# Optimization experiments

Hardware: AMD Instinct MI355X
Metric: run time of the kernel (lower is better)

Reference implementation:

```python
import jax, jax.numpy as jnp
import numpy as np

H_HEADS = 8
DIM_HEAD = 64


def setup_inputs() -> dict:
    key = jax.random.key(0)
    ks = jax.random.split(key, 5)
    b, c, Hs, Ws = 16, 32, 128, 128
    qd = H_HEADS * c              # 256 (heads*c = Linear in_features)
    inner = H_HEADS * DIM_HEAD    # 512
    s = 0.02                      # keep logits in a sane range
    return {
        "x": jax.random.normal(ks[0], (b, c, Hs, Ws), jnp.float32),
        "Wq": jax.random.normal(ks[1], (inner, qd), jnp.float32) * s,
        "Wkv": jax.random.normal(ks[2], (2 * inner, qd), jnp.float32) * s,
        "Wout": jax.random.normal(ks[3], (qd, inner), jnp.float32) * s,
        "bout": jax.random.normal(ks[4], (qd,), jnp.float32) * s,
    }


def _proj(arg, W, bias=None):
    # apply_operator_or_ffn for nn.Linear:
    # rearrange '(b h) n d -> b d (h n)', Linear over last dim, then 'b d n -> b n d'
    B, n, d = arg.shape
    bp = B // H_HEADS
    t = arg.reshape(bp, H_HEADS, n, d)
    t = jnp.transpose(t, (0, 3, 1, 2)).reshape(bp, d, H_HEADS * n)  # [b', d, h*n]
    y = t @ W.T
    if bias is not None:
        y = y + bias
    return jnp.transpose(y, (0, 2, 1))  # [b', out_features, d]


def _split_heads(t):
    # 'b (h d) n -> (b h) d n'
    bp, hd, n = t.shape
    return t.reshape(bp, H_HEADS, hd // H_HEADS, n).reshape(bp * H_HEADS, hd // H_HEADS, n)


def reference(x, Wq, Wkv, Wout, bout):
    b, c = x.shape[0], x.shape[1]
    spatial = x.shape[2:]
    N = int(np.prod(spatial))
    scale = DIM_HEAD ** -0.5
    xf = x.reshape(b, c, N)
    q = _proj(xf, Wq)              # [b/h, inner, N]
    kv = _proj(xf, Wkv)            # [b/h, 2*inner, N]
    inner = q.shape[1]
    k, v = kv[:, :inner], kv[:, inner:]
    qh, kh, vh = _split_heads(q), _split_heads(k), _split_heads(v)  # [b, DIM_HEAD, N]
    sim = jnp.einsum('bin,bjn->bij', qh, kh) * scale                 # [b, dh, dh]
    attn = jax.nn.softmax(sim, axis=-1)
    out = jnp.einsum('bnj,bjd->bnd', attn, vh)                       # [b, dh, N]
    out = _proj(out, Wout, bout)                                     # [b/h, h*c, N]
    return out.reshape(b, c, *spatial)
```

## Files before the change

### kernel.cpp

```cpp
#include <hip/hip_runtime.h>
#include <cstdint>
#include <cstddef>

using u16 = unsigned short;
using u32 = unsigned int;

typedef __attribute__((ext_vector_type(8))) short bf16x8;
typedef __attribute__((ext_vector_type(16))) float f32x16;

__device__ __forceinline__ u16 f2bf(float f) {
  union { float f; u32 i; } x; x.f = f;
  u32 r = (x.i + 0x7FFFu + ((x.i >> 16) & 1u)) >> 16;
  return (u16)r;
}
__device__ __forceinline__ bf16x8 ldbf16x8(const u16* p) {
  union { uint4 u; bf16x8 v; } t;
  t.u = *(const uint4*)p;
  return t.v;
}

constexpr int NP = 16384;

constexpr size_t OFF_C   = 0;
constexpr size_t OFF_T   = 131072;
constexpr size_t OFF_AT  = 393216;
constexpr size_t OFF_WE  = 458752;
constexpr size_t OFF_MT  = 720896;
constexpr size_t OFF_MA  = 851968;
constexpr size_t OFF_XB  = 917504;
constexpr size_t OFF_XBT = 5111808;
constexpr size_t OFF_CP1 = 9306112;
constexpr size_t NEED1   = (OFF_CP1 + 2097152) * 4;
constexpr size_t OFF_CP2 = 851968;
constexpr size_t NEED2   = (OFF_CP2 + 6291456) * 4;

__global__ __launch_bounds__(256)
void k0_cvt(const float* __restrict__ x, u16* __restrict__ Xb,
            u16* __restrict__ XbT) {
  __shared__ float Fs[256 * 65];
  const int pc = blockIdx.x;
  const int g  = blockIdx.y;
  const int p0 = pc * 64;
  const float* __restrict__ Xg = x + (size_t)g * 256 * NP;
  u16* __restrict__ Xbg  = Xb  + (size_t)g * 256 * NP;
  u16* __restrict__ XbTg = XbT + (size_t)g * NP * 256;
  const int tid = threadIdx.x;
  const int f8i = tid & 7, rb = tid >> 3;
  for (int pass = 0; pass < 8; ++pass) {
    const int row = rb + pass * 32;
    const size_t e0 = (size_t)row * NP + p0 + f8i * 8;
    float4 a = *(const float4*)(Xg + e0);
    float4 b = *(const float4*)(Xg + e0 + 4);
    const float v[8] = {a.x, a.y, a.z, a.w, b.x, b.y, b.z, b.w};
    uint4 s;
    s.x = (u32)f2bf(v[0]) | ((u32)f2bf(v[1]) << 16);
    s.y = (u32)f2bf(v[2]) | ((u32)f2bf(v[3]) << 16);
    s.z = (u32)f2bf(v[4]) | ((u32)f2bf(v[5]) << 16);
    s.w = (u32)f2bf(v[6]) | ((u32)f2bf(v[7]) << 16);
    *(uint4*)(Xbg + e0) = s;
    float* d = &Fs[row * 65 + f8i * 8];
#pragma unroll
    for (int e = 0; e < 8; ++e) d[e] = v[e];
  }
  __syncthreads();
  const int p = tid & 63, grp = tid >> 6;
  u16* dst = XbTg + (size_t)(p0 + p) * 256 + grp * 64;
  for (int c = 0; c < 4; ++c) {
    u32 w[8];
#pragma unroll
    for (int q = 0; q < 8; ++q) {
      const int f = grp * 64 + c * 16 + q * 2;
      u32 lo = f2bf(Fs[f * 65 + p]);
      u32 hi = f2bf(Fs[(f + 1) * 65 + p]);
      w[q] = lo | (hi << 16);
    }
    uint4 s0 = {w[0], w[1], w[2], w[3]};
    uint4 s1 = {w[4], w[5], w[6], w[7]};
    *(uint4*)(dst + c * 16)     = s0;
    *(uint4*)(dst + c * 16 + 8) = s1;
  }
}

__global__ __launch_bounds__(256)
void k1_mfma(const u16* __restrict__ Xb, float* __restrict__ Cpart) {
  const int kc = blockIdx.x;
  const int tp = blockIdx.y;
  const int g  = blockIdx.z;
  const int ti = tp >> 2, tj = tp & 3;
  const int tid = threadIdx.x;
  const int w = tid >> 6, half = (tid >> 5) & 1, lc = tid & 31;
  const int qi = w >> 1, qj = w & 1;
  const u16* __restrict__ Xg = Xb + (size_t)g * 256 * NP;
  const u16* A = Xg + (size_t)(ti * 64 + qi * 32 + lc) * NP + kc * 1024 + half * 8;
  const u16* B = Xg + (size_t)(tj * 64 + qj * 32 + lc) * NP + kc * 1024 + half * 8;
  f32x16 acc;
#pragma unroll
  for (int i = 0; i < 16; ++i) acc[i] = 0.f;
#pragma unroll 4
  for (int s = 0; s < 64; ++s) {
    bf16x8 a = ldbf16x8(A + s * 16);
    bf16x8 b = ldbf16x8(B + s * 16);
    acc = __builtin_amdgcn_mfma_f32_32x32x16_bf16(a, b, acc, 0, 0, 0);
  }
  float* __restrict__ P = Cpart + (((size_t)g * 16 + tp) * 16 + kc) * 4096;
#pragma unroll
  for (int r = 0; r < 16; ++r) {
    const int row = qi * 32 + (r & 3) + 8 * (r >> 2) + 4 * half;
    const int col = qj * 32 + lc;
    P[row * 64 + col] = acc[r];
  }
}

__global__ __launch_bounds__(256)
void k1b_red(const float* __restrict__ Cpart, float* __restrict__ Cmat) {
  const int sl = blockIdx.x;
  const int tp = blockIdx.y;
  const int g  = blockIdx.z;
  const int ele = sl * 256 + threadIdx.x;
  const float* __restrict__ P =
      Cpart + (((size_t)g * 16 + tp) * 16) * 4096 + ele;
  float v = 0.f;
#pragma unroll
  for (int kc = 0; kc < 16; ++kc) v += P[(size_t)kc * 4096];
  const int ti = tp >> 2, tj = tp & 3;
  const int r64 = ele >> 6, c64 = ele & 63;
  Cmat[(size_t)g * 65536 + (size_t)(ti * 64 + r64) * 256 + tj * 64 + c64] = v;
}

__global__ __launch_bounds__(256)
void k1_gram(const float* __restrict__ x, float* __restrict__ Cpart) {
  __shared__ float As[32 * 132];
  __shared__ float Bs[32 * 132];
  const int kc = blockIdx.x, ty = blockIdx.y, g = blockIdx.z;
  const int i0 = (ty == 2) ? 128 : 0;
  const int j0 = (ty == 0) ? 0 : 128;
  const float* __restrict__ Xg = x + (size_t)g * 256 * NP;
  const int tid = threadIdx.x, lane = tid & 63, w = tid >> 6;
  const int wy = (w >> 1) * 64, wx = (w & 1) * 64;
  const int ly = (lane >> 3) * 8, lx = (lane & 7) * 8;
  float acc[8][8];
#pragma unroll
  for (int e = 0; e < 8; ++e)
#pragma unroll
    for (int f = 0; f < 8; ++f) acc[e][f] = 0.f;
  const int k8 = (tid & 3) * 8, rowb = tid >> 2, k0 = kc * 256;
  for (int s = 0; s < 8; ++s) {
    const int ks = k0 + s * 32;
#pragma unroll
    for (int pass = 0; pass < 2; ++pass) {
      const int row = rowb + pass * 64;
      const size_t ea = (size_t)(i0 + row) * NP + ks + k8;
      float4 a = *(const float4*)(Xg + ea);
      float4 b = *(const float4*)(Xg + ea + 4);
      As[(k8+0)*132+row]=a.x; As[(k8+1)*132+row]=a.y;
      As[(k8+2)*132+row]=a.z; As[(k8+3)*132+row]=a.w;
      As[(k8+4)*132+row]=b.x; As[(k8+5)*132+row]=b.y;
      As[(k8+6)*132+row]=b.z; As[(k8+7)*132+row]=b.w;
      const size_t eb = (size_t)(j0 + row) * NP + ks + k8;
      a = *(const float4*)(Xg + eb);
      b = *(const float4*)(Xg + eb + 4);
      Bs[(k8+0)*132+row]=a.x; Bs[(k8+1)*132+row]=a.y;
      Bs[(k8+2)*132+row]=a.z; Bs[(k8+3)*132+row]=a.w;
      Bs[(k8+4)*132+row]=b.x; Bs[(k8+5)*132+row]=b.y;
      Bs[(k8+6)*132+row]=b.z; Bs[(k8+7)*132+row]=b.w;
    }
    __syncthreads();
#pragma unroll 4
    for (int kk = 0; kk < 32; ++kk) {
      const float* ar = &As[kk * 132 + wy + ly];
      const float* br = &Bs[kk * 132 + wx + lx];
      float4 a0 = *(const float4*)(ar), a1 = *(const float4*)(ar + 4);
      float4 b0 = *(const float4*)(br), b1 = *(const float4*)(br + 4);
      const float av[8] = {a0.x,a0.y,a0.z,a0.w,a1.x,a1.y,a1.z,a1.w};
      const float bv[8] = {b0.x,b0.y,b0.z,b0.w,b1.x,b1.y,b1.z,b1.w};
#pragma unroll
      for (int e = 0; e < 8; ++e)
#pragma unroll
        for (int f = 0; f < 8; ++f) acc[e][f] += av[e] * bv[f];
    }
    __syncthreads();
  }
  float* __restrict__ P = Cpart + (((size_t)g * 3 + ty) * 64 + kc) * 16384;
#pragma unroll
  for (int e = 0; e < 8; ++e) {
    float* pr = P + (size_t)(wy + ly + e) * 128 + wx + lx;
    float4 s0 = {acc[e][0], acc[e][1], acc[e][2], acc[e][3]};
    float4 s1 = {acc[e][4], acc[e][5], acc[e][6], acc[e][7]};
    *(float4*)(pr)     = s0;
    *(float4*)(pr + 4) = s1;
  }
}

__global__ __launch_bounds__(256)
void k1b_reduce(const float* __restrict__ Cpart, float* __restrict__ Cmat) {
  const int sl = blockIdx.x, ty = blockIdx.y, g = blockIdx.z;
  const int ele = sl * 256 + threadIdx.x;
  const float* __restrict__ P =
      Cpart + (((size_t)g * 3 + ty) * 64) * 16384 + ele;
  float v = 0.f;
#pragma unroll 8
  for (int kc = 0; kc < 64; ++kc) v += P[(size_t)kc * 16384];
  const int i0 = (ty == 2) ? 128 : 0;
  const int j0 = (ty == 0) ? 0 : 128;
  const int i = ele >> 7, j = ele & 127;
  float* Cg = Cmat + (size_t)g * 65536;
  Cg[(size_t)(i0 + i) * 256 + (j0 + j)] = v;
  if (ty == 1) Cg[(size_t)(j0 + j) * 256 + (i0 + i)] = v;
}

__global__ __launch_bounds__(256)
void k1_gram_atomic(const float* __restrict__ x, float* __restrict__ Cmat) {
  __shared__ float As[32 * 132];
  __shared__ float Bs[32 * 132];
  const int kc = blockIdx.x, ty = blockIdx.y, g = blockIdx.z;
  const int i0 = (ty == 2) ? 128 : 0;
  const int j0 = (ty == 0) ? 0 : 128;
  const float* __restrict__ Xg = x + (size_t)g * 256 * NP;
  const int tid = threadIdx.x, lane = tid & 63, w = tid >> 6;
  const int wy = (w >> 1) * 64, wx = (w & 1) * 64;
  const int ly = (lane >> 3) * 8, lx = (lane & 7) * 8;
  float acc[8][8];
#pragma unroll
  for (int e = 0; e < 8; ++e)
#pragma unroll
    for (int f = 0; f < 8; ++f) acc[e][f] = 0.f;
  const int k8 = (tid & 3) * 8, rowb = tid >> 2, k0 = kc * 256;
  for (int s = 0; s < 8; ++s) {
    const int ks = k0 + s * 32;
#pragma unroll
    for (int pass = 0; pass < 2; ++pass) {
      const int row = rowb + pass * 64;
      const size_t ea = (size_t)(i0 + row) * NP + ks + k8;
      float4 a = *(const float4*)(Xg + ea);
      float4 b = *(const float4*)(Xg + ea + 4);
      As[(k8+0)*132+row]=a.x; As[(k8+1)*132+row]=a.y;
      As[(k8+2)*132+row]=a.z; As[(k8+3)*132+row]=a.w;
      As[(k8+4)*132+row]=b.x; As[(k8+5)*132+row]=b.y;
      As[(k8+6)*132+row]=b.z; As[(k8+7)*132+row]=b.w;
      const size_t eb = (size_t)(j0 + row) * NP + ks + k8;
      a = *(const float4*)(Xg + eb);
      b = *(const float4*)(Xg + eb + 4);
      Bs[(k8+0)*132+row]=a.x; Bs[(k8+1)*132+row]=a.y;
      Bs[(k8+2)*132+row]=a.z; Bs[(k8+3)*132+row]=a.w;
      Bs[(k8+4)*132+row]=b.x; Bs[(k8+5)*132+row]=b.y;
      Bs[(k8+6)*132+row]=b.z; Bs[(k8+7)*132+row]=b.w;
    }
    __syncthreads();
#pragma unroll 4
    for (int kk = 0; kk < 32; ++kk) {
      const float* ar = &As[kk * 132 + wy + ly];
      const float* br = &Bs[kk * 132 + wx + lx];
      float4 a0 = *(const float4*)(ar), a1 = *(const float4*)(ar + 4);
      float4 b0 = *(const float4*)(br), b1 = *(const float4*)(br + 4);
      const float av[8] = {a0.x,a0.y,a0.z,a0.w,a1.x,a1.y,a1.z,a1.w};
      const float bv[8] = {b0.x,b0.y,b0.z,b0.w,b1.x,b1.y,b1.z,b1.w};
#pragma unroll
      for (int e = 0; e < 8; ++e)
#pragma unroll
        for (int f = 0; f < 8; ++f) acc[e][f] += av[e] * bv[f];
    }
    __syncthreads();
  }
  float* Cg = Cmat + (size_t)g * 65536;
#pragma unroll
  for (int e = 0; e < 8; ++e)
#pragma unroll
    for (int f = 0; f < 8; ++f) {
      atomicAdd(&Cg[(i0+wy+ly+e)*256 + (j0+wx+lx+f)], acc[e][f]);
      if (ty == 1)
        atomicAdd(&Cg[(j0+wx+lx+f)*256 + (i0+wy+ly+e)], acc[e][f]);
    }
}

__global__ __launch_bounds__(256)
void kA_attn(const float* __restrict__ Wq, const float* __restrict__ Wkv,
             const float* __restrict__ Cmat, float* __restrict__ attn) {
  __shared__ float WqL[4 * 256];
  __shared__ float Ts[4 * 256];
  const int bh = blockIdx.x;
  const int ic = blockIdx.y;
  const int g = bh >> 3, hh = bh & 7;
  const int tid = threadIdx.x;
  const float* __restrict__ Cg = Cmat + (size_t)g * 65536;
  {
    const int r = tid >> 6, c4 = (tid & 63) * 4;
    *(float4*)(&WqL[r * 256 + c4]) =
        *(const float4*)(Wq + (size_t)(hh * 64 + ic * 4 + r) * 256 + c4);
  }
  __syncthreads();
  float acc[4] = {0.f, 0.f, 0.f, 0.f};
#pragma unroll 8
  for (int b = 0; b < 256; ++b) {
    const float cv = Cg[(size_t)b * 256 + tid];
#pragma unroll
    for (int r = 0; r < 4; ++r) acc[r] += WqL[r * 256 + b] * cv;
  }
#pragma unroll
  for (int r = 0; r < 4; ++r) Ts[r * 256 + tid] = acc[r];
  __syncthreads();
  const int r = tid >> 6, j = tid & 63;
  const float* __restrict__ Wk = Wkv + (size_t)(hh * 64 + j) * 256;
  float s = 0.f;
#pragma unroll 4
  for (int a4 = 0; a4 < 64; ++a4) {
    float4 w = *(const float4*)(Wk + a4 * 4);
    const float* t4 = &Ts[r * 256 + a4 * 4];
    s += t4[0] * w.x + t4[1] * w.y + t4[2] * w.z + t4[3] * w.w;
  }
  s *= 0.125f;
  float m = s;
#pragma unroll
  for (int off = 32; off; off >>= 1) m = fmaxf(m, __shfl_xor(m, off));
  const float e = __expf(s - m);
  float sum = e;
#pragma unroll
  for (int off = 32; off; off >>= 1) sum += __shfl_xor(sum, off);
  attn[((size_t)bh * 64 + ic * 4 + r) * 64 + j] = e / sum;
}

__global__ __launch_bounds__(256)
void kB_m(const float* __restrict__ Wout, const float* __restrict__ Wkv,
          const float* __restrict__ attn, float* __restrict__ Mp) {
  __shared__ float AtL[64 * 64];
  __shared__ float WoL[16 * 64];
  __shared__ float UL[16 * 64];
  const int bh = blockIdx.x;
  const int cc = blockIdx.y;
  const int g = bh >> 3, hh = bh & 7;
  const int tid = threadIdx.x;
  {
    const float* __restrict__ A = attn + (size_t)bh * 4096;
#pragma unroll
    for (int q = 0; q < 4; ++q)
      *(float4*)(&AtL[q * 1024 + tid * 4]) =
          *(const float4*)(A + q * 1024 + tid * 4);
  }
  {
    const int co_l = tid >> 4, i4 = (tid & 15) * 4;
    *(float4*)(&WoL[co_l * 64 + i4]) =
        *(const float4*)(Wout + (size_t)(cc * 16 + co_l) * 512 + hh * 64 + i4);
  }
  __syncthreads();
  const int j = tid & 63, cw = tid >> 6;
  float u4[4] = {0.f, 0.f, 0.f, 0.f};
#pragma unroll 4
  for (int i = 0; i < 64; ++i) {
    const float av = AtL[i * 64 + j];
#pragma unroll
    for (int u = 0; u < 4; ++u) u4[u] += WoL[(cw * 4 + u) * 64 + i] * av;
  }
  __syncthreads();
#pragma unroll
  for (int u = 0; u < 4; ++u) UL[(cw * 4 + u) * 64 + j] = u4[u];
  __syncthreads();
  float acc[16];
#pragma unroll
  for (int c = 0; c < 16; ++c) acc[c] = 0.f;
#pragma unroll 4
  for (int j2 = 0; j2 < 64; ++j2) {
    const float wv = Wkv[(size_t)(512 + hh * 64 + j2) * 256 + tid];
#pragma unroll
    for (int c = 0; c < 16; ++c) acc[c] += UL[c * 64 + j2] * wv;
  }
  float* __restrict__ P =
      Mp + (((size_t)g * 8 + hh) * 256 + cc * 16) * 256 + tid;
#pragma unroll
  for (int c = 0; c < 16; ++c) P[(size_t)c * 256] = acc[c];
}

__global__ __launch_bounds__(256)
void kC_red(const float* __restrict__ Mp, u16* __restrict__ MA) {
  const int co = blockIdx.x;
  const int g  = blockIdx.y;
  const int b  = threadIdx.x;
  const float* __restrict__ P = Mp + ((size_t)g * 8 * 256 + co) * 256 + b;
  float v = 0.f;
#pragma unroll
  for (int h = 0; h < 8; ++h) v += P[(size_t)h * 65536];
  MA[((size_t)g * 256 + co) * 256 + b] = f2bf(v);
}

__global__ __launch_bounds__(256) void k2_T(const float* __restrict__ Wq,
                                            const float* __restrict__ Cmat,
                                            float* __restrict__ T) {
  const int bh = blockIdx.x;
  const int ic = blockIdx.y;
  const int g = bh >> 3, hh = bh & 7;
  const int tid = threadIdx.x;
  const float* __restrict__ Cg = Cmat + (size_t)g * 65536;
  const int r0 = hh * 64 + ic * 4;
  float acc[4] = {0.f, 0.f, 0.f, 0.f};
#pragma unroll 8
  for (int b = 0; b < 256; ++b) {
    const float cv = Cg[(size_t)b * 256 + tid];
#pragma unroll
    for (int ii = 0; ii < 4; ++ii)
      acc[ii] += Wq[(size_t)(r0 + ii) * 256 + b] * cv;
  }
#pragma unroll
  for (int ii = 0; ii < 4; ++ii)
    T[((size_t)bh * 64 + ic * 4 + ii) * 256 + tid] = acc[ii];
}

__global__ __launch_bounds__(256) void k3_sim(const float* __restrict__ Wkv,
                                              const float* __restrict__ T,
                                              float* __restrict__ simattn) {
  __shared__ float Ts[64 * 256];
  const int bh = blockIdx.x;
  const int jc = blockIdx.y;
  const int hh = bh & 7;
  const int tid = threadIdx.x;
  {
    const int f4i = tid & 63;
    const int rwb = tid >> 6;
    for (int pass = 0; pass < 16; ++pass) {
      const int row = rwb + pass * 4;
      float4 v = *(const float4*)(T + ((size_t)bh * 64 + row) * 256 + f4i * 4);
      const int a0 = f4i * 4;
      const float vv[4] = {v.x, v.y, v.z, v.w};
#pragma unroll
      for (int e = 0; e < 4; ++e) {
        const int a = a0 + e;
        Ts[row * 256 + (a & ~31) + ((a + row) & 31)] = vv[e];
      }
    }
  }
  __syncthreads();
  const int i  = tid & 63;
  const int jq = tid >> 6;
  const int jb = jc * 16 + jq * 4;
  float acc[4] = {0.f, 0.f, 0.f, 0.f};
#pragma unroll 4
  for (int a = 0; a < 256; ++a) {
    const float tv = Ts[i * 256 + (a & ~31) + ((a + i) & 31)];
#pragma unroll
    for (int jj = 0; jj < 4; ++jj)
      acc[jj] += Wkv[(size_t)(hh * 64 + jb + jj) * 256 + a] * tv;
  }
#pragma unroll
  for (int jj = 0; jj < 4; ++jj)
    simattn[((size_t)bh * 64 + i) * 64 + jb + jj] = acc[jj] * 0.125f;
}

__global__ __launch_bounds__(64) void k3b_softmax(float* __restrict__ simattn) {
  const int bh = blockIdx.x;
  const int i  = threadIdx.x;
  float* row = simattn + ((size_t)bh * 64 + i) * 64;
  float v[64];
  float m = -1e30f;
#pragma unroll
  for (int j = 0; j < 64; ++j) { v[j] = row[j]; m = fmaxf(m, v[j]); }
  float s = 0.f;
#pragma unroll
  for (int j = 0; j < 64; ++j) { v[j] = __expf(v[j] - m); s += v[j]; }
  const float inv = 1.0f / s;
#pragma unroll
  for (int j = 0; j < 64; ++j) row[j] = v[j] * inv;
}

__global__ __launch_bounds__(256) void k4_we(const float* __restrict__ Wout,
                                             const float* __restrict__ attn,
                                             float* __restrict__ WeT) {
  __shared__ float WL[256 * 64];
  const int jc = blockIdx.x;
  const int hh = blockIdx.y;
  const int g  = blockIdx.z;
  const int bh = g * 8 + hh;
  const int tid = threadIdx.x;
  {
    const int f4i = tid & 15;
    const int cb  = tid >> 4;
    for (int pass = 0; pass < 16; ++pass) {
      const int co = cb + pass * 16;
      float4 v = *(const float4*)(Wout + (size_t)co * 512 + hh * 64 + f4i * 4);
      const int a0 = f4i * 4;
      const float vv[4] = {v.x, v.y, v.z, v.w};
#pragma unroll
      for (int e = 0; e < 4; ++e)
        WL[co * 64 + ((a0 + e + co) & 63)] = vv[e];
    }
  }
  __syncthreads();
  const int jb = jc * 8;
  float acc[8] = {0.f, 0.f, 0.f, 0.f, 0.f, 0.f, 0.f, 0.f};
#pragma unroll 4
  for (int i = 0; i < 64; ++i) {
    const float wv = WL[tid * 64 + ((i + tid) & 63)];
#pragma unroll
    for (int je = 0; je < 8; ++je)
      acc[je] += attn[((size_t)bh * 64 + i) * 64 + jb + je] * wv;
  }
#pragma unroll
  for (int je = 0; je < 8; ++je)
    WeT[(size_t)g * 131072 + (size_t)(hh * 64 + jb + je) * 256 + tid] =
        acc[je];
}

__global__ __launch_bounds__(256)
void k5a_part(const float* __restrict__ Wkv, const float* __restrict__ WeT,
              float* __restrict__ Mp) {
  const int bc = blockIdx.x;
  const int oc = blockIdx.y;
  const int g  = blockIdx.z;
  const int tid = threadIdx.x;
  const int b0 = bc * 4;
  const float* __restrict__ Weg = WeT + (size_t)g * 131072;
  float acc[4] = {0.f, 0.f, 0.f, 0.f};
#pragma unroll 8
  for (int u = 0; u < 32; ++u) {
    const int o = oc * 32 + u;
    const float wv = Weg[(size_t)o * 256 + tid];
    const float* __restrict__ vr = Wkv + (size_t)(512 + o) * 256 + b0;
    acc[0] += vr[0] * wv;
    acc[1] += vr[1] * wv;
    acc[2] += vr[2] * wv;
    acc[3] += vr[3] * wv;
  }
#pragma unroll
  for (int be = 0; be < 4; ++be)
    Mp[(((size_t)g * 16 + oc) * 256 + b0 + be) * 256 + tid] = acc[be];
}

__global__ __launch_bounds__(256)
void k5b_red(const float* __restrict__ Mp, float* __restrict__ Mt,
             u16* __restrict__ MA) {
  const int b = blockIdx.x;
  const int g = blockIdx.y;
  const int tid = threadIdx.x;
  const float* __restrict__ P =
      Mp + ((size_t)g * 16 * 256 + b) * 256 + tid;
  float v = 0.f;
#pragma unroll
  for (int oc = 0; oc < 16; ++oc) v += P[(size_t)oc * 65536];
  Mt[(size_t)g * 65536 + (size_t)b * 256 + tid] = v;
  MA[(size_t)g * 65536 + (size_t)tid * 256 + b] = f2bf(v);
}

__global__ __launch_bounds__(256) void k5_serial(const float* __restrict__ Wkv,
                                                 const float* __restrict__ WeT,
                                                 float* __restrict__ Mt,
                                                 u16* __restrict__ MA) {
  const int bc = blockIdx.x;
  const int g  = blockIdx.y;
  const int tid = threadIdx.x;
  const int b0 = bc * 4;
  const float* __restrict__ Weg = WeT + (size_t)g * 131072;
  float acc[4] = {0.f, 0.f, 0.f, 0.f};
#pragma unroll 4
  for (int o = 0; o < 512; ++o) {
    const float wv = Weg[(size_t)o * 256 + tid];
    const float* __restrict__ vr = Wkv + (size_t)(512 + o) * 256 + b0;
    acc[0] += vr[0] * wv;
    acc[1] += vr[1] * wv;
    acc[2] += vr[2] * wv;
    acc[3] += vr[3] * wv;
  }
#pragma unroll
  for (int be = 0; be < 4; ++be) {
    Mt[(size_t)g * 65536 + (size_t)(b0 + be) * 256 + tid] = acc[be];
    MA[(size_t)g * 65536 + (size_t)tid * 256 + b0 + be] = f2bf(acc[be]);
  }
}

__global__ __launch_bounds__(256)
void k6_mfma(const u16* __restrict__ XbT, const u16* __restrict__ MA,
             const float* __restrict__ bout, float* __restrict__ out) {
  const int pb = blockIdx.x;
  const int cb = blockIdx.y;
  const int g  = blockIdx.z;
  const int tid = threadIdx.x;
  const int w = tid >> 6, half = (tid >> 5) & 1, lc = tid & 31;
  const int p0  = pb * 128 + w * 32;
  const int co0 = cb * 128;
  const u16* __restrict__ Ap =
      XbT + ((size_t)g * NP + p0 + lc) * 256 + half * 8;
  const u16* __restrict__ Mg = MA + (size_t)g * 65536;
  f32x16 acc[4];
#pragma unroll
  for (int t = 0; t < 4; ++t)
#pragma unroll
    for (int i = 0; i < 16; ++i) acc[t][i] = 0.f;
#pragma unroll 2
  for (int s = 0; s < 16; ++s) {
    bf16x8 a = ldbf16x8(Ap + s * 16);
#pragma unroll
    for (int t = 0; t < 4; ++t) {
      bf16x8 b =
          ldbf16x8(Mg + (size_t)(co0 + t * 32 + lc) * 256 + half * 8 + s * 16);
      acc[t] = __builtin_amdgcn_mfma_f32_32x32x16_bf16(a, b, acc[t], 0, 0, 0);
    }
  }
#pragma unroll
  for (int t = 0; t < 4; ++t) {
    const int co = co0 + t * 32 + lc;
    const float bo = bout[co];
    float* __restrict__ ocol =
        out + ((size_t)(g * 256 + co)) * NP + p0 + 4 * half;
#pragma unroll
    for (int rg = 0; rg < 4; ++rg) {
      float4 v = {acc[t][rg * 4 + 0] + bo, acc[t][rg * 4 + 1] + bo,
                  acc[t][rg * 4 + 2] + bo, acc[t][rg * 4 + 3] + bo};
      *(float4*)(ocol + rg * 8) = v;
    }
  }
}

__global__ __launch_bounds__(256)
void k6_apply(const float* __restrict__ x, const float* __restrict__ Mt,
              const float* __restrict__ bout, float* __restrict__ out) {
  __shared__ float As[32 * 132];
  __shared__ float Bs[32 * 132];
  const int pc = blockIdx.x;
  const int oy = blockIdx.y;
  const int g  = blockIdx.z;
  const int p0 = pc * 128;
  const int o0 = oy * 128;
  const float* __restrict__ Xg = x + (size_t)g * 256 * NP;
  const float* __restrict__ Mg = Mt + (size_t)g * 65536;
  const int tid  = threadIdx.x;
  const int lane = tid & 63;
  const int w    = tid >> 6;
  const int wy = (w >> 1) * 64;
  const int wx = (w & 1) * 64;
  const int ly = (lane >> 3) * 8;
  const int lx = (lane & 7) * 8;
  float acc[8][8];
#pragma unroll
  for (int e = 0; e < 8; ++e)
#pragma unroll
    for (int f = 0; f < 8; ++f) acc[e][f] = 0.f;
  const int c4 = (tid & 31) * 4;
  const int kb = tid >> 5;
  for (int s = 0; s < 8; ++s) {
#pragma unroll
    for (int r = 0; r < 4; ++r) {
      const int kk = kb + r * 8;
      const int f  = s * 32 + kk;
      *(float4*)&As[kk * 132 + c4] =
          *(const float4*)(Mg + (size_t)f * 256 + o0 + c4);
      *(float4*)&Bs[kk * 132 + c4] =
          *(const float4*)(Xg + (size_t)f * NP + p0 + c4);
    }
    __syncthreads();
#pragma unroll 4
    for (int kk = 0; kk < 32; ++kk) {
      const float* __restrict__ ar = &As[kk * 132 + wy + ly];
      const float* __restrict__ br = &Bs[kk * 132 + wx + lx];
      float4 a0 = *(const float4*)(ar);
      float4 a1 = *(const float4*)(ar + 4);
      float4 b0 = *(const float4*)(br);
      float4 b1 = *(const float4*)(br + 4);
      const float av[8] = {a0.x, a0.y, a0.z, a0.w, a1.x, a1.y, a1.z, a1.w};
      const float bv[8] = {b0.x, b0.y, b0.z, b0.w, b1.x, b1.y, b1.z, b1.w};
#pragma unroll
      for (int e = 0; e < 8; ++e)
#pragma unroll
        for (int f = 0; f < 8; ++f) acc[e][f] += av[e] * bv[f];
    }
    __syncthreads();
  }
#pragma unroll
  for (int e = 0; e < 8; ++e) {
    const int co = o0 + wy + ly + e;
    const float bo = bout[co];
    float* __restrict__ orow =
        out + ((size_t)(g * 256 + co)) * NP + p0 + wx + lx;
    float4 s0 = {acc[e][0] + bo, acc[e][1] + bo, acc[e][2] + bo,
                 acc[e][3] + bo};
    float4 s1 = {acc[e][4] + bo, acc[e][5] + bo, acc[e][6] + bo,
                 acc[e][7] + bo};
    *(float4*)(orow)     = s0;
    *(float4*)(orow + 4) = s1;
  }
}

extern "C" void kernel_launch(void* const* d_in, const int* in_sizes, int n_in,
                              void* d_out, int out_size, void* d_ws,
                              size_t ws_size, hipStream_t stream) {
  const float* x    = (const float*)d_in[0];
  const float* Wq   = (const float*)d_in[1];
  const float* Wkv  = (const float*)d_in[2];
  const float* Wout = (const float*)d_in[3];
  const float* bout = (const float*)d_in[4];
  float* out = (float*)d_out;
  float* ws  = (float*)d_ws;

  float* C    = ws + OFF_C;
  float* T    = ws + OFF_T;
  float* att  = ws + OFF_AT;
  float* WeT  = ws + OFF_WE;
  float* Mt   = ws + OFF_MT;
  u16*   MA   = (u16*)(ws + OFF_MA);
  u16*   Xb   = (u16*)(ws + OFF_XB);
  u16*   XbT  = (u16*)(ws + OFF_XBT);
  float* Cp1  = ws + OFF_CP1;
  float* Cp2  = ws + OFF_CP2;

  const bool mfma_path = (ws_size >= NEED1);
  const bool splitk    = (ws_size >= NEED2);

  if (mfma_path) {
    k0_cvt<<<dim3(256, 2), 256, 0, stream>>>(x, Xb, XbT);
    k1_mfma<<<dim3(16, 16, 2), 256, 0, stream>>>(Xb, Cp1);
    k1b_red<<<dim3(16, 16, 2), 256, 0, stream>>>(Cp1, C);
    kA_attn<<<dim3(16, 16), 256, 0, stream>>>(Wq, Wkv, C, att);
    kB_m<<<dim3(16, 16), 256, 0, stream>>>(Wout, Wkv, att, Cp1);
    kC_red<<<dim3(256, 2), 256, 0, stream>>>(Cp1, MA);
    k6_mfma<<<dim3(128, 2, 2), 256, 0, stream>>>(XbT, MA, bout, out);
    return;
  }

  if (splitk) {
    k1_gram<<<dim3(64, 3, 2), 256, 0, stream>>>(x, Cp2);
    k1b_reduce<<<dim3(64, 3, 2), 256, 0, stream>>>(Cp2, C);
  } else {
    hipMemsetAsync(C, 0, 131072 * sizeof(float), stream);
    k1_gram_atomic<<<dim3(64, 3, 2), 256, 0, stream>>>(x, C);
  }
  k2_T<<<dim3(16, 16), 256, 0, stream>>>(Wq, C, T);
  k3_sim<<<dim3(16, 4), 256, 0, stream>>>(Wkv, T, att);
  k3b_softmax<<<dim3(16), 64, 0, stream>>>(att);
  k4_we<<<dim3(8, 8, 2), 256, 0, stream>>>(Wout, att, WeT);
  if (splitk) {
    k5a_part<<<dim3(64, 16, 2), 256, 0, stream>>>(Wkv, WeT, Cp2);
    k5b_red<<<dim3(256, 2), 256, 0, stream>>>(Cp2, Mt, MA);
  } else {
    k5_serial<<<dim3(64, 2), 256, 0, stream>>>(Wkv, WeT, Mt, MA);
  }
  k6_apply<<<dim3(128, 2, 2), 256, 0, stream>>>(x, Mt, bout, out);
}
```

Baseline: 184.0 us.

## Store bf16 operands in MFMA-fragment panel layout for coalesced loads

The conversion kernel now writes the bf16 copies of x (and its transpose) in a panel-blocked layout where each 32-row panel stores k-steps contiguously, so each wave's MFMA operand load is a contiguous 512-element chunk instead of a strided row read. The Gram MFMA kernel, the output MFMA kernel and the reduction that produces MA are rewritten to use this layout; the MA reduction now writes whole 8-element vectors with fewer blocks. This targets uncoalesced global loads in the MFMA kernels, at the cost of scattered writes in the conversion kernel and a reduction kernel with much less parallelism.

```diff
diff --git a/kernel.cpp b/kernel.cpp
--- a/kernel.cpp
+++ b/kernel.cpp
@@ -20,6 +20,7 @@
 }
 
 constexpr int NP = 16384;
+
 
 constexpr size_t OFF_C   = 0;
 constexpr size_t OFF_T   = 131072;
@@ -35,17 +36,19 @@
 constexpr size_t NEED2   = (OFF_CP2 + 6291456) * 4;
 
 __global__ __launch_bounds__(256)
-void k0_cvt(const float* __restrict__ x, u16* __restrict__ Xb,
-            u16* __restrict__ XbT) {
+void k0_cvt(const float* __restrict__ x, u16* __restrict__ XbF,
+            u16* __restrict__ XbTF) {
   __shared__ float Fs[256 * 65];
   const int pc = blockIdx.x;
   const int g  = blockIdx.y;
   const int p0 = pc * 64;
   const float* __restrict__ Xg = x + (size_t)g * 256 * NP;
-  u16* __restrict__ Xbg  = Xb  + (size_t)g * 256 * NP;
-  u16* __restrict__ XbTg = XbT + (size_t)g * NP * 256;
+  u16* __restrict__ XbFg  = XbF  + (size_t)g * 256 * NP;
+  u16* __restrict__ XbTFg = XbTF + (size_t)g * NP * 256;
   const int tid = threadIdx.x;
   const int f8i = tid & 7, rb = tid >> 3;
+  const int sA = pc * 4 + (f8i >> 1);
+  const int hA = f8i & 1;
   for (int pass = 0; pass < 8; ++pass) {
     const int row = rb + pass * 32;
     const size_t e0 = (size_t)row * NP + p0 + f8i * 8;
@@ -57,15 +60,19 @@
     s.y = (u32)f2bf(v[2]) | ((u32)f2bf(v[3]) << 16);
     s.z = (u32)f2bf(v[4]) | ((u32)f2bf(v[5]) << 16);
     s.w = (u32)f2bf(v[6]) | ((u32)f2bf(v[7]) << 16);
-    *(uint4*)(Xbg + e0) = s;
+    const int panel = row >> 5, lc = row & 31;
+    *(uint4*)(XbFg + (size_t)panel * 524288 + sA * 512 + hA * 256 + lc * 8) = s;
     float* d = &Fs[row * 65 + f8i * 8];
 #pragma unroll
     for (int e = 0; e < 8; ++e) d[e] = v[e];
   }
   __syncthreads();
   const int p = tid & 63, grp = tid >> 6;
-  u16* dst = XbTg + (size_t)(p0 + p) * 256 + grp * 64;
+  const int pp = p0 + p;
+  const int panelT = pp >> 5, lcT = pp & 31;
+  u16* dstT = XbTFg + (size_t)panelT * 8192 + lcT * 8;
   for (int c = 0; c < 4; ++c) {
+    const int sT = grp * 4 + c;
     u32 w[8];
 #pragma unroll
     for (int q = 0; q < 8; ++q) {
@@ -76,13 +83,13 @@
     }
     uint4 s0 = {w[0], w[1], w[2], w[3]};
     uint4 s1 = {w[4], w[5], w[6], w[7]};
-    *(uint4*)(dst + c * 16)     = s0;
-    *(uint4*)(dst + c * 16 + 8) = s1;
-  }
-}
-
-__global__ __launch_bounds__(256)
-void k1_mfma(const u16* __restrict__ Xb, float* __restrict__ Cpart) {
+    *(uint4*)(dstT + sT * 512)       = s0;
+    *(uint4*)(dstT + sT * 512 + 256) = s1;
+  }
+}
+
+__global__ __launch_bounds__(256)
+void k1_mfma(const u16* __restrict__ XbF, float* __restrict__ Cpart) {
   const int kc = blockIdx.x;
   const int tp = blockIdx.y;
   const int g  = blockIdx.z;
@@ -90,16 +97,18 @@
   const int tid = threadIdx.x;
   const int w = tid >> 6, half = (tid >> 5) & 1, lc = tid & 31;
   const int qi = w >> 1, qj = w & 1;
-  const u16* __restrict__ Xg = Xb + (size_t)g * 256 * NP;
-  const u16* A = Xg + (size_t)(ti * 64 + qi * 32 + lc) * NP + kc * 1024 + half * 8;
-  const u16* B = Xg + (size_t)(tj * 64 + qj * 32 + lc) * NP + kc * 1024 + half * 8;
+  const u16* __restrict__ Xg = XbF + (size_t)g * 256 * NP;
+  const u16* A = Xg + (size_t)(ti * 2 + qi) * 524288 + (size_t)kc * 32768 +
+                 half * 256 + lc * 8;
+  const u16* B = Xg + (size_t)(tj * 2 + qj) * 524288 + (size_t)kc * 32768 +
+                 half * 256 + lc * 8;
   f32x16 acc;
 #pragma unroll
   for (int i = 0; i < 16; ++i) acc[i] = 0.f;
 #pragma unroll 4
   for (int s = 0; s < 64; ++s) {
-    bf16x8 a = ldbf16x8(A + s * 16);
-    bf16x8 b = ldbf16x8(B + s * 16);
+    bf16x8 a = ldbf16x8(A + s * 512);
+    bf16x8 b = ldbf16x8(B + s * 512);
     acc = __builtin_amdgcn_mfma_f32_32x32x16_bf16(a, b, acc, 0, 0, 0);
   }
   float* __restrict__ P = Cpart + (((size_t)g * 16 + tp) * 16 + kc) * 4096;
@@ -370,14 +379,33 @@
 
 __global__ __launch_bounds__(256)
 void kC_red(const float* __restrict__ Mp, u16* __restrict__ MA) {
-  const int co = blockIdx.x;
-  const int g  = blockIdx.y;
-  const int b  = threadIdx.x;
-  const float* __restrict__ P = Mp + ((size_t)g * 8 * 256 + co) * 256 + b;
-  float v = 0.f;
-#pragma unroll
-  for (int h = 0; h < 8; ++h) v += P[(size_t)h * 65536];
-  MA[((size_t)g * 256 + co) * 256 + b] = f2bf(v);
+  const int panel = blockIdx.x;
+  const int g     = blockIdx.y;
+  const int tid = threadIdx.x;
+  const float* __restrict__ Pg = Mp + (size_t)g * 8 * 65536;
+  u16* __restrict__ Mg = MA + (size_t)g * 65536;
+#pragma unroll
+  for (int q = 0; q < 4; ++q) {
+    const int item = tid + q * 256;
+    const int lc = item & 31;
+    const int co = panel * 32 + lc;
+    const int b0 = (item >> 5) * 8;
+    float v[8] = {0.f, 0.f, 0.f, 0.f, 0.f, 0.f, 0.f, 0.f};
+#pragma unroll
+    for (int hd = 0; hd < 8; ++hd) {
+      const float* p = Pg + (size_t)hd * 65536 + (size_t)co * 256 + b0;
+      float4 a = *(const float4*)(p);
+      float4 b = *(const float4*)(p + 4);
+      v[0] += a.x; v[1] += a.y; v[2] += a.z; v[3] += a.w;
+      v[4] += b.x; v[5] += b.y; v[6] += b.z; v[7] += b.w;
+    }
+    uint4 sdat;
+    sdat.x = (u32)f2bf(v[0]) | ((u32)f2bf(v[1]) << 16);
+    sdat.y = (u32)f2bf(v[2]) | ((u32)f2bf(v[3]) << 16);
+    sdat.z = (u32)f2bf(v[4]) | ((u32)f2bf(v[5]) << 16);
+    sdat.w = (u32)f2bf(v[6]) | ((u32)f2bf(v[7]) << 16);
+    *(uint4*)(Mg + (size_t)panel * 8192 + (size_t)item * 8) = sdat;
+  }
 }
 
 __global__ __launch_bounds__(256) void k2_T(const float* __restrict__ Wq,
@@ -563,7 +591,7 @@
 }
 
 __global__ __launch_bounds__(256)
-void k6_mfma(const u16* __restrict__ XbT, const u16* __restrict__ MA,
+void k6_mfma(const u16* __restrict__ XbTF, const u16* __restrict__ MA,
              const float* __restrict__ bout, float* __restrict__ out) {
   const int pb = blockIdx.x;
   const int cb = blockIdx.y;
@@ -572,9 +600,11 @@
   const int w = tid >> 6, half = (tid >> 5) & 1, lc = tid & 31;
   const int p0  = pb * 128 + w * 32;
   const int co0 = cb * 128;
-  const u16* __restrict__ Ap =
-      XbT + ((size_t)g * NP + p0 + lc) * 256 + half * 8;
-  const u16* __restrict__ Mg = MA + (size_t)g * 65536;
+  const u16* __restrict__ Ap = XbTF + (size_t)g * NP * 256 +
+                               (size_t)(pb * 4 + w) * 8192 + half * 256 +
+                               lc * 8;
+  const u16* __restrict__ Bp = MA + (size_t)g * 65536 +
+                               (size_t)cb * 32768 + half * 256 + lc * 8;
   f32x16 acc[4];
 #pragma unroll
   for (int t = 0; t < 4; ++t)
@@ -582,11 +612,10 @@
     for (int i = 0; i < 16; ++i) acc[t][i] = 0.f;
 #pragma unroll 2
   for (int s = 0; s < 16; ++s) {
-    bf16x8 a = ldbf16x8(Ap + s * 16);
+    bf16x8 a = ldbf16x8(Ap + s * 512);
 #pragma unroll
     for (int t = 0; t < 4; ++t) {
-      bf16x8 b =
-          ldbf16x8(Mg + (size_t)(co0 + t * 32 + lc) * 256 + half * 8 + s * 16);
+      bf16x8 b = ldbf16x8(Bp + (size_t)t * 8192 + s * 512);
       acc[t] = __builtin_amdgcn_mfma_f32_32x32x16_bf16(a, b, acc[t], 0, 0, 0);
     }
   }
@@ -705,7 +734,7 @@
     k1b_red<<<dim3(16, 16, 2), 256, 0, stream>>>(Cp1, C);
     kA_attn<<<dim3(16, 16), 256, 0, stream>>>(Wq, Wkv, C, att);
     kB_m<<<dim3(16, 16), 256, 0, stream>>>(Wout, Wkv, att, Cp1);
-    kC_red<<<dim3(256, 2), 256, 0, stream>>>(Cp1, MA);
+    kC_red<<<dim3(8, 2), 256, 0, stream>>>(Cp1, MA);
     k6_mfma<<<dim3(128, 2, 2), 256, 0, stream>>>(XbT, MA, bout, out);
     return;
   }
```

Measured after the change: 158.8 us. 1.16x faster.
